# Optimization experiments

Measured on AMD Instinct MI355X. Metric: run time of the kernel, lower is better.

## Reference

```python
import jax, jax.numpy as jnp
import numpy as np

K = 16            # top-k negatives kept per row
TEMP = 0.01       # softmax temperature
V = 0.95          # geometric decay base
NEG_FILL = -1e9   # masks out same-class entries before topk (never selected since k << #negatives)


def _l2norm(x):
    # torch F.normalize: x / max(||x||, eps)
    n = jnp.linalg.norm(x, axis=-1, keepdims=True)
    return x / jnp.maximum(n, 1e-12)


def setup_inputs() -> dict:
    key = jax.random.key(0)
    k1, k2, k3 = jax.random.split(key, 3)
    feature = jax.random.normal(k1, (4096, 128), dtype=jnp.float32)
    negative_features = jax.random.normal(k2, (4, 4096, 128), dtype=jnp.float32)
    target = jax.random.randint(k3, (4096,), 0, 4)
    return {"feature": feature, "target": target,
            "negative_features": negative_features, "idx": 0}


def reference(feature, target, negative_features, idx):
    J = negative_features.shape[0]
    f = _l2norm(feature)                       # [n, d]
    negs = _l2norm(negative_features)          # [J, n, d]
    # cosine similarity for every negative set: [J, n, n]
    sims = jnp.einsum('nd,jmd->jnm', f, negs)
    # same-class mask, applied only to the idx-th set
    same = target[:, None] == target[None, :]  # [n, n]
    sims = sims.at[idx].set(jnp.where(same, NEG_FILL, sims[idx]))
    # per-row top-k over the last (candidate) dim: [J, n, K]
    top, _ = jax.lax.top_k(sims, K)
    logits = jnp.transpose(top, (1, 0, 2)) / TEMP   # [n, J, K]
    p = jax.nn.softmax(logits, axis=1)
    logp = jax.nn.log_softmax(logits, axis=1)
    ent = jnp.sum(p * logp, axis=1)                 # [n, K]
    decay = V ** jnp.arange(K, dtype=jnp.float32)
    decay = decay / jnp.sum(decay)                  # L1-normalized, matches F.normalize(p=1)
    loss = jnp.mean(jnp.sum(ent * decay, axis=1)) + jnp.log(jnp.float32(J))
    return loss
```

## Files before the change

### kernel.cpp

```cpp
#include <hip/hip_runtime.h>
#include <hip/hip_bf16.h>
#include <math.h>

#define N 4096
#define D 128
#define NJ 4
#define KTOP 16
#define CSPLIT 2

typedef __attribute__((ext_vector_type(8))) short bf16x8;
typedef __attribute__((ext_vector_type(4))) float f32x4;


__device__ __forceinline__ void bitonic_sort16_desc(float* a) {
    #pragma unroll
    for (int k = 2; k <= 16; k <<= 1) {
        #pragma unroll
        for (int jj = k >> 1; jj > 0; jj >>= 1) {
            #pragma unroll
            for (int i = 0; i < 16; i++) {
                int l = i ^ jj;
                if (l > i) {
                    bool up = ((i & k) == 0);
                    float x = a[i], y = a[l];
                    float mx = fmaxf(x, y), mn = fminf(x, y);
                    a[i] = up ? mx : mn;
                    a[l] = up ? mn : mx;
                }
            }
        }
    }
}

__device__ __forceinline__ void bitonic_clean16_desc(float* a) {
    #pragma unroll
    for (int jj = 8; jj > 0; jj >>= 1) {
        #pragma unroll
        for (int i = 0; i < 16; i++) {
            int l = i ^ jj;
            if (l > i) {
                float x = a[i], y = a[l];
                a[i] = fmaxf(x, y);
                a[l] = fminf(x, y);
            }
        }
    }
}

__global__ __launch_bounds__(256) void neguni_prep(
    const float* __restrict__ feat, const float* __restrict__ negs,
    unsigned short* __restrict__ fh, unsigned short* __restrict__ gh)
{
    __shared__ __align__(16) float fraw[64 * 132];
    __shared__ __align__(16) unsigned short obuf[8192];

    const int t = threadIdx.x;
    const int b = blockIdx.x;
    const bool is_f = (b < 64);

    const float4* src = is_f ? ((const float4*)feat) + (size_t)b * 2048
                             : ((const float4*)negs) + (size_t)(b - 64) * 2048;
    float4* frawv = (float4*)fraw;
    #pragma unroll
    for (int i = 0; i < 8; i++) {
        const int g = i * 256 + t;
        frawv[(g >> 5) * 33 + (g & 31)] = src[g];
    }
    __syncthreads();

    const int row_l = t >> 2;
    const int s     = t & 3;
    float4 v[8];
    #pragma unroll
    for (int k = 0; k < 8; k++) v[k] = frawv[row_l * 33 + s * 8 + k];

    float ss = 0.f;
    #pragma unroll
    for (int k = 0; k < 8; k++)
        ss += v[k].x * v[k].x + v[k].y * v[k].y + v[k].z * v[k].z + v[k].w * v[k].w;
    ss += __shfl_xor(ss, 1, 64);
    ss += __shfl_xor(ss, 2, 64);
    const float inv = 1.0f / fmaxf(sqrtf(ss), 1e-12f);

    const int tt  = row_l >> 4;
    const int col = row_l & 15;
    uint4* obufv = (uint4*)obuf;
    #pragma unroll
    for (int q = 0; q < 4; q++) {
        float fe[8] = {v[q*2].x, v[q*2].y, v[q*2].z, v[q*2].w,
                       v[q*2+1].x, v[q*2+1].y, v[q*2+1].z, v[q*2+1].w};
        unsigned int u[4];
        #pragma unroll
        for (int i = 0; i < 4; i++) {
            __hip_bfloat16 b0 = __float2bfloat16(fe[2*i]   * inv);
            __hip_bfloat16 b1 = __float2bfloat16(fe[2*i+1] * inv);
            u[i] = ((unsigned int)*(unsigned short*)&b1 << 16) | *(unsigned short*)&b0;
        }
        uint4 pk; pk.x = u[0]; pk.y = u[1]; pk.z = u[2]; pk.w = u[3];
        const int pos = is_f ? (row_l * 16 + s * 4 + q)
                             : ((s * 4 + tt) * 64 + q * 16 + col);
        obufv[pos] = pk;
    }
    __syncthreads();

    uint4* dst;
    if (is_f) {
        dst = ((uint4*)fh) + (size_t)b * 1024;
    } else {
        const int bn  = b - 64;
        const int j   = bn >> 6;
        const int chg = bn & 63;
        dst = ((uint4*)(gh + (size_t)j * N * D)) + (size_t)chg * 1024;
    }
    #pragma unroll
    for (int i = 0; i < 4; i++) dst[i * 256 + t] = obufv[i * 256 + t];
}

__global__ __launch_bounds__(256) void neguni_main(
    const unsigned short* __restrict__ fh, const unsigned short* __restrict__ gh,
    const int* __restrict__ target, const int* __restrict__ idxp,
    float* __restrict__ topbuf)
{
    __shared__ float tops[4][16][17];

    const int tid   = threadIdx.x;
    const int w     = tid >> 6;
    const int lane  = tid & 63;
    const int col16 = lane & 15;
    const int quad  = lane >> 4;

    const int j   = blockIdx.x & 3;
    const int ft  = (blockIdx.x >> 2) & 255;
    const int cs  = blockIdx.x >> 10;
    const int r0  = ft * 16;
    const int c0  = cs * 2048 + w * 512;
    const int idx = idxp[0];
    const bool msk = (j == idx);

    bf16x8 bfr[4];
    {
        const unsigned short* fr = fh + (size_t)(r0 + col16) * D + quad * 8;
        bfr[0] = *(const bf16x8*)(fr);
        bfr[1] = *(const bf16x8*)(fr + 32);
        bfr[2] = *(const bf16x8*)(fr + 64);
        bfr[3] = *(const bf16x8*)(fr + 96);
    }
    const int rtg = target[r0 + col16];

    float lst[KTOP];

    const int chg0 = cs * 32 + w * 8;
    const unsigned short* ab0 = gh + (size_t)j * N * D + (size_t)chg0 * 8192 + lane * 8;

    #pragma unroll 1
    for (int ch = 0; ch < 8; ch++) {
        const unsigned short* ab = ab0 + (size_t)ch * 8192;

        f32x4 acc[4];
        #pragma unroll
        for (int t = 0; t < 4; t++) acc[t] = (f32x4){0.f, 0.f, 0.f, 0.f};

        #pragma unroll
        for (int s = 0; s < 4; s++) {
            #pragma unroll
            for (int t = 0; t < 4; t++) {
                bf16x8 a = *(const bf16x8*)(ab + (s * 4 + t) * 512);
                acc[t] = __builtin_amdgcn_mfma_f32_16x16x32_bf16(a, bfr[s], acc[t], 0, 0, 0);
            }
        }

        const int cbase = c0 + ch * 64;
        float s16[16];
        #pragma unroll
        for (int t = 0; t < 4; t++) {
            s16[t * 4 + 0] = acc[t][0];
            s16[t * 4 + 1] = acc[t][1];
            s16[t * 4 + 2] = acc[t][2];
            s16[t * 4 + 3] = acc[t][3];
        }
        if (msk) {
            #pragma unroll
            for (int t = 0; t < 4; t++) {
                int4 tc = *(const int4*)(target + cbase + t * 16 + quad * 4);
                if (tc.x == rtg) s16[t * 4 + 0] = -1e9f;
                if (tc.y == rtg) s16[t * 4 + 1] = -1e9f;
                if (tc.z == rtg) s16[t * 4 + 2] = -1e9f;
                if (tc.w == rtg) s16[t * 4 + 3] = -1e9f;
            }
        }

        bitonic_sort16_desc(s16);
        if (ch == 0) {
            #pragma unroll
            for (int i = 0; i < 16; i++) lst[i] = s16[i];
        } else {
            float mg[16];
            #pragma unroll
            for (int i = 0; i < 16; i++) mg[i] = fmaxf(lst[i], s16[15 - i]);
            bitonic_clean16_desc(mg);
            #pragma unroll
            for (int i = 0; i < 16; i++) lst[i] = mg[i];
        }
    }

    #pragma unroll
    for (int off = 16; off <= 32; off <<= 1) {
        float mg[16];
        #pragma unroll
        for (int i = 0; i < 16; i++)
            mg[i] = fmaxf(lst[i], __shfl_xor(lst[15 - i], off, 64));
        bitonic_clean16_desc(mg);
        #pragma unroll
        for (int i = 0; i < 16; i++) lst[i] = mg[i];
    }

    if (lane < 16) {
        #pragma unroll
        for (int i = 0; i < 16; i++) tops[w][lane][i] = lst[i];
        tops[w][lane][16] = -3.0e38f;
    }
    __syncthreads();

    if (tid < 16) {
        int i0 = 0, i1 = 0, i2 = 0, i3 = 0;
        float* outp = topbuf + (((size_t)j * N + r0 + tid) * CSPLIT + cs) * KTOP;
        #pragma unroll
        for (int k = 0; k < KTOP; k++) {
            float v0 = tops[0][tid][i0], v1 = tops[1][tid][i1];
            float v2 = tops[2][tid][i2], v3 = tops[3][tid][i3];
            float m01 = fmaxf(v0, v1), m23 = fmaxf(v2, v3);
            float mx  = fmaxf(m01, m23);
            if      (mx == v0) i0++;
            else if (mx == v1) i1++;
            else if (mx == v2) i2++;
            else               i3++;
            outp[k] = mx;
        }
    }
}

__global__ __launch_bounds__(256) void neguni_fin(
    const float* __restrict__ topbuf, float* __restrict__ out)
{
    __shared__ float buf[256][35];
    __shared__ float mm[64][65];
    __shared__ float red[4];

    const int t     = threadIdx.x;
    const int j     = t >> 6;
    const int row_l = t & 63;
    const int row   = blockIdx.x * 64 + row_l;

    const float4* src = (const float4*)(topbuf + ((size_t)j * N + row) * (CSPLIT * KTOP));
    #pragma unroll
    for (int q = 0; q < 8; q++) {
        float4 v = src[q];
        const int base = (q >> 2) * 17 + (q & 3) * 4;
        buf[t][base + 0] = v.x;
        buf[t][base + 1] = v.y;
        buf[t][base + 2] = v.z;
        buf[t][base + 3] = v.w;
    }
    buf[t][16] = -3.0e38f;
    buf[t][33] = -3.0e38f;

    {
        int ia = 0, ib = 17;
        #pragma unroll
        for (int k = 0; k < KTOP; k++) {
            float va = buf[t][ia], vb = buf[t][ib];
            bool ta = va >= vb;
            mm[row_l][k * 4 + j] = ta ? va : vb;
            if (ta) ia++; else ib++;
        }
    }
    __syncthreads();

    float val = 0.f;
    const float Ssum = (1.0f - powf(0.95f, 16.0f)) / 0.05f;
    #pragma unroll
    for (int i = 0; i < 4; i++) {
        const int idx = t + i * 256;
        const int rl  = idx & 63;
        const int k   = idx >> 6;
        float l0 = mm[rl][k * 4 + 0] * 100.0f;
        float l1 = mm[rl][k * 4 + 1] * 100.0f;
        float l2 = mm[rl][k * 4 + 2] * 100.0f;
        float l3 = mm[rl][k * 4 + 3] * 100.0f;
        float m  = fmaxf(fmaxf(l0, l1), fmaxf(l2, l3));
        float d0 = l0 - m, d1 = l1 - m, d2 = l2 - m, d3 = l3 - m;
        float e0 = expf(d0), e1 = expf(d1), e2 = expf(d2), e3 = expf(d3);
        float s  = e0 + e1 + e2 + e3;
        float ent = (e0 * d0 + e1 * d1 + e2 * d2 + e3 * d3) / s - logf(s);
        val += ent * powf(0.95f, (float)k);
    }
    val *= 1.0f / (Ssum * (float)N);

    #pragma unroll
    for (int off = 32; off > 0; off >>= 1) val += __shfl_xor(val, off, 64);
    if ((t & 63) == 0) red[t >> 6] = val;
    __syncthreads();
    if (t == 0) atomicAdd(out, red[0] + red[1] + red[2] + red[3]);
    if (blockIdx.x == 0 && t == 0) atomicAdd(out, logf(4.0f));
}

extern "C" void kernel_launch(void* const* d_in, const int* in_sizes, int n_in,
                              void* d_out, int out_size, void* d_ws, size_t ws_size,
                              hipStream_t stream) {
    const float* feat   = (const float*)d_in[0];
    const int*   target = (const int*)d_in[1];
    const float* negs   = (const float*)d_in[2];
    const int*   idxp   = (const int*)d_in[3];
    float* out = (float*)d_out;

    unsigned short* fh = (unsigned short*)d_ws;
    unsigned short* gh = fh + (size_t)N * D;
    float* topbuf      = (float*)(gh + (size_t)NJ * N * D);

    hipMemsetAsync(out, 0, sizeof(float), stream);
    neguni_prep<<<dim3((N + NJ * N) / 64), dim3(256), 0, stream>>>(feat, negs, fh, gh);
    neguni_main<<<dim3(NJ * (N / 16) * CSPLIT), dim3(256), 0, stream>>>(fh, gh, target, idxp, topbuf);
    neguni_fin<<<dim3(N / 64), dim3(256), 0, stream>>>(topbuf, out);
}
```

Baseline: 136.6 us.

## Fuse final reduction into main kernel via last-block atomic counter

Removes the separate finalize kernel and the memset by having the last of the eight blocks per 16-row tile (tracked with an atomic counter) merge the partial top-k lists and compute the entropy contribution. Zeroing of the output and counters moves into the prep kernel. This saves two launches and a pass over the top-k buffer, but adds a threadfence, an atomic per block, and a tail of serial merge work in the winning blocks.

```diff
diff --git a/kernel.cpp b/kernel.cpp
--- a/kernel.cpp
+++ b/kernel.cpp
@@ -49,7 +49,8 @@
 
 __global__ __launch_bounds__(256) void neguni_prep(
     const float* __restrict__ feat, const float* __restrict__ negs,
-    unsigned short* __restrict__ fh, unsigned short* __restrict__ gh)
+    unsigned short* __restrict__ fh, unsigned short* __restrict__ gh,
+    int* __restrict__ cnt, float* __restrict__ out)
 {
     __shared__ __align__(16) float fraw[64 * 132];
     __shared__ __align__(16) unsigned short obuf[8192];
@@ -57,6 +58,11 @@
     const int t = threadIdx.x;
     const int b = blockIdx.x;
     const bool is_f = (b < 64);
+
+    if (b == 0) {
+        if (t == 0) out[0] = 0.f;
+        cnt[t] = 0;
+    }
 
     const float4* src = is_f ? ((const float4*)feat) + (size_t)b * 2048
                              : ((const float4*)negs) + (size_t)(b - 64) * 2048;
@@ -119,9 +125,13 @@
 __global__ __launch_bounds__(256) void neguni_main(
     const unsigned short* __restrict__ fh, const unsigned short* __restrict__ gh,
     const int* __restrict__ target, const int* __restrict__ idxp,
-    float* __restrict__ topbuf)
+    float* __restrict__ topbuf, int* __restrict__ cnt, float* __restrict__ out)
 {
     __shared__ float tops[4][16][17];
+    __shared__ float fbuf[64][35];
+    __shared__ float mm[16][65];
+    __shared__ float red[4];
+    __shared__ int winflag;
 
     const int tid   = threadIdx.x;
     const int w     = tid >> 6;
@@ -237,71 +247,65 @@
             outp[k] = mx;
         }
     }
-}
-
-__global__ __launch_bounds__(256) void neguni_fin(
-    const float* __restrict__ topbuf, float* __restrict__ out)
-{
-    __shared__ float buf[256][35];
-    __shared__ float mm[64][65];
-    __shared__ float red[4];
-
-    const int t     = threadIdx.x;
-    const int j     = t >> 6;
-    const int row_l = t & 63;
-    const int row   = blockIdx.x * 64 + row_l;
-
-    const float4* src = (const float4*)(topbuf + ((size_t)j * N + row) * (CSPLIT * KTOP));
-    #pragma unroll
-    for (int q = 0; q < 8; q++) {
-        float4 v = src[q];
-        const int base = (q >> 2) * 17 + (q & 3) * 4;
-        buf[t][base + 0] = v.x;
-        buf[t][base + 1] = v.y;
-        buf[t][base + 2] = v.z;
-        buf[t][base + 3] = v.w;
-    }
-    buf[t][16] = -3.0e38f;
-    buf[t][33] = -3.0e38f;
+    __syncthreads();
+
+    if (tid == 0) {
+        __threadfence();
+        int old = atomicAdd(&cnt[ft], 1);
+        winflag = (old == 7) ? 1 : 0;
+    }
+    __syncthreads();
+    if (!winflag) return;
+
+    __threadfence();
+    if (tid < 64) {
+        const int jj = tid >> 4;
+        const int rr = tid & 15;
+        const float* srcp = topbuf + (((size_t)jj * N + r0 + rr) * CSPLIT) * KTOP;
+        #pragma unroll
+        for (int q = 0; q < 16; q++)
+            fbuf[tid][q] = __hip_atomic_load(srcp + q, __ATOMIC_RELAXED, __HIP_MEMORY_SCOPE_AGENT);
+        #pragma unroll
+        for (int q = 0; q < 16; q++)
+            fbuf[tid][17 + q] = __hip_atomic_load(srcp + 16 + q, __ATOMIC_RELAXED, __HIP_MEMORY_SCOPE_AGENT);
+        fbuf[tid][16] = -3.0e38f;
+        fbuf[tid][33] = -3.0e38f;
+        int ia = 0, ib = 17;
+        #pragma unroll
+        for (int k = 0; k < KTOP; k++) {
+            float va = fbuf[tid][ia], vb = fbuf[tid][ib];
+            bool ta = va >= vb;
+            mm[rr][k * 4 + jj] = ta ? va : vb;
+            if (ta) ia++; else ib++;
+        }
+    }
+    __syncthreads();
 
     {
-        int ia = 0, ib = 17;
-        #pragma unroll
-        for (int k = 0; k < KTOP; k++) {
-            float va = buf[t][ia], vb = buf[t][ib];
-            bool ta = va >= vb;
-            mm[row_l][k * 4 + j] = ta ? va : vb;
-            if (ta) ia++; else ib++;
-        }
-    }
-    __syncthreads();
-
-    float val = 0.f;
-    const float Ssum = (1.0f - powf(0.95f, 16.0f)) / 0.05f;
-    #pragma unroll
-    for (int i = 0; i < 4; i++) {
-        const int idx = t + i * 256;
-        const int rl  = idx & 63;
-        const int k   = idx >> 6;
-        float l0 = mm[rl][k * 4 + 0] * 100.0f;
-        float l1 = mm[rl][k * 4 + 1] * 100.0f;
-        float l2 = mm[rl][k * 4 + 2] * 100.0f;
-        float l3 = mm[rl][k * 4 + 3] * 100.0f;
+        const int rr = tid >> 4;
+        const int k  = tid & 15;
+        const float Ssum = (1.0f - powf(0.95f, 16.0f)) / 0.05f;
+        float l0 = mm[rr][k * 4 + 0] * 100.0f;
+        float l1 = mm[rr][k * 4 + 1] * 100.0f;
+        float l2 = mm[rr][k * 4 + 2] * 100.0f;
+        float l3 = mm[rr][k * 4 + 3] * 100.0f;
         float m  = fmaxf(fmaxf(l0, l1), fmaxf(l2, l3));
         float d0 = l0 - m, d1 = l1 - m, d2 = l2 - m, d3 = l3 - m;
         float e0 = expf(d0), e1 = expf(d1), e2 = expf(d2), e3 = expf(d3);
         float s  = e0 + e1 + e2 + e3;
         float ent = (e0 * d0 + e1 * d1 + e2 * d2 + e3 * d3) / s - logf(s);
-        val += ent * powf(0.95f, (float)k);
-    }
-    val *= 1.0f / (Ssum * (float)N);
-
-    #pragma unroll
-    for (int off = 32; off > 0; off >>= 1) val += __shfl_xor(val, off, 64);
-    if ((t & 63) == 0) red[t >> 6] = val;
-    __syncthreads();
-    if (t == 0) atomicAdd(out, red[0] + red[1] + red[2] + red[3]);
-    if (blockIdx.x == 0 && t == 0) atomicAdd(out, logf(4.0f));
+        float val = ent * powf(0.95f, (float)k) / (Ssum * (float)N);
+
+        #pragma unroll
+        for (int off = 32; off > 0; off >>= 1) val += __shfl_xor(val, off, 64);
+        if ((tid & 63) == 0) red[tid >> 6] = val;
+    }
+    __syncthreads();
+    if (tid == 0) {
+        float tot = red[0] + red[1] + red[2] + red[3];
+        if (ft == 0) tot += logf(4.0f);
+        atomicAdd(out, tot);
+    }
 }
 
 extern "C" void kernel_launch(void* const* d_in, const int* in_sizes, int n_in,
@@ -316,9 +320,8 @@
     unsigned short* fh = (unsigned short*)d_ws;
     unsigned short* gh = fh + (size_t)N * D;
     float* topbuf      = (float*)(gh + (size_t)NJ * N * D);
-
-    hipMemsetAsync(out, 0, sizeof(float), stream);
-    neguni_prep<<<dim3((N + NJ * N) / 64), dim3(256), 0, stream>>>(feat, negs, fh, gh);
-    neguni_main<<<dim3(NJ * (N / 16) * CSPLIT), dim3(256), 0, stream>>>(fh, gh, target, idxp, topbuf);
-    neguni_fin<<<dim3(N / 64), dim3(256), 0, stream>>>(topbuf, out);
-}
+    int*   cnt         = (int*)(topbuf + (size_t)NJ * N * CSPLIT * KTOP);
+
+    neguni_prep<<<dim3((N + NJ * N) / 64), dim3(256), 0, stream>>>(feat, negs, fh, gh, cnt, out);
+    neguni_main<<<dim3(NJ * (N / 16) * CSPLIT), dim3(256), 0, stream>>>(fh, gh, target, idxp, topbuf, cnt, out);
+}
```

Measured after the change: 306.6 us. 2.24x slower.
